# Kernel tuning notes

Measured on AMD Instinct MI355X. Metric: run time of the kernel, lower is better.

The kernel has to match this reference:

```python
import jax, jax.numpy as jnp
import numpy as np

B, N, D, H, HID = 8, 729, 1152, 12, 4304
HD = D // H
EPS = 1e-6


def _layer_norm(x, g, b):
    mu = jnp.mean(x, axis=-1, keepdims=True)
    var = jnp.mean((x - mu) ** 2, axis=-1, keepdims=True)
    return (x - mu) / jnp.sqrt(var + EPS) * g + b


def setup_inputs() -> dict:
    key = jax.random.key(0)
    ks = jax.random.split(key, 9)
    s = 0.02
    return {
        "x": jax.random.normal(ks[0], (B, N, D), jnp.float32),
        "wq": jax.random.normal(ks[1], (D, D), jnp.float32) * s,
        "bq": jnp.zeros((D,), jnp.float32),
        "wk": jax.random.normal(ks[2], (D, D), jnp.float32) * s,
        "bk": jnp.zeros((D,), jnp.float32),
        "wv": jax.random.normal(ks[3], (D, D), jnp.float32) * s,
        "bv": jnp.zeros((D,), jnp.float32),
        "wo": jax.random.normal(ks[4], (D, D), jnp.float32) * s,
        "bo": jnp.zeros((D,), jnp.float32),
        "ln1_g": jnp.ones((D,), jnp.float32),
        "ln1_b": jnp.zeros((D,), jnp.float32),
        "w_fc1": jax.random.normal(ks[5], (HID, D), jnp.float32) * s,
        "b_fc1": jnp.zeros((HID,), jnp.float32),
        "w_fc2": jax.random.normal(ks[6], (D, HID), jnp.float32) * s,
        "b_fc2": jnp.zeros((D,), jnp.float32),
        "ln2_g": jnp.ones((D,), jnp.float32),
        "ln2_b": jnp.zeros((D,), jnp.float32),
    }


def reference(x, wq, bq, wk, bk, wv, bv, wo, bo, ln1_g, ln1_b,
              w_fc1, b_fc1, w_fc2, b_fc2, ln2_g, ln2_b):
    b, n, d = x.shape
    # split_heads in the source is a plain view (B, H, N, HD) -- NOT a transpose.
    def heads(t):
        return t.reshape(b, H, n, HD)

    Q = heads(x @ wq.T + bq)
    K = heads(x @ wk.T + bk)
    V = heads(x @ wv.T + bv)

    scores = jnp.einsum("bhqd,bhkd->bhqk", Q, K) * (HD ** -0.5)
    attn_w = jax.nn.softmax(scores, axis=-1)
    o = jnp.einsum("bhqk,bhkd->bhqd", attn_w, V)  # [B,H,N,HD]
    o = jnp.swapaxes(o, 1, 2).reshape(b, n, d)
    attn_out = o @ wo.T + bo

    # post-norm: LN(sublayer) + residual
    h = _layer_norm(attn_out, ln1_g, ln1_b) + x

    # quirky MLP: activation applied BEFORE fc1 (faithful to source)
    m = jax.nn.gelu(h, approximate=True)
    m = m @ w_fc1.T + b_fc1
    m = m @ w_fc2.T + b_fc2

    return _layer_norm(m, ln2_g, ln2_b) + h
```

## Files before the change

### kernel.cpp

```cpp
#include <hip/hip_runtime.h>
#include <hip/hip_bf16.h>

#define BF16 __hip_bfloat16

typedef short short8 __attribute__((ext_vector_type(8)));
typedef short short4v __attribute__((ext_vector_type(4)));
typedef float v4f __attribute__((ext_vector_type(4)));
typedef float f4 __attribute__((ext_vector_type(4)));

__device__ float g_bp[1152];
__device__ BF16  g_wm[1152 * 1152];

__device__ __forceinline__ short f2bs(float f) {
    __hip_bfloat16 h = __float2bfloat16(f);
    return *(short*)&h;
}

__device__ __forceinline__ float bs2f(short s) {
    __hip_bfloat16 h = *(__hip_bfloat16*)&s;
    return __bfloat162float(h);
}

__device__ __forceinline__ void async_cp16(const BF16* g, BF16* l) {
    __builtin_amdgcn_global_load_lds(
        (const __attribute__((address_space(1))) void*)g,
        (__attribute__((address_space(3))) void*)l,
        16, 0, 0);
}

__global__ __launch_bounds__(256) void prep_kernel(
    const float* __restrict__ wq, const float* __restrict__ wk,
    const float* __restrict__ wv, const float* __restrict__ wo,
    const float* __restrict__ wfc1, const float* __restrict__ wfc2,
    const float* __restrict__ x,
    const float* __restrict__ bfc1, const float* __restrict__ bfc2,
    BF16* __restrict__ wbq, BF16* __restrict__ wbk,
    BF16* __restrict__ wbv, BF16* __restrict__ wbo,
    BF16* __restrict__ wbf1t, BF16* __restrict__ wbf2,
    BF16* __restrict__ xb)
{
    __shared__ float tile[64][65];
    const int bid = blockIdx.x;
    const int tid = threadIdx.x;

    if (bid < 16641) {
        const int i = bid * 256 + tid;
        constexpr int N_DD  = 331776;
        constexpr int N4    = 4 * N_DD;
        constexpr int N_F2  = 1253376;
        constexpr int E_F2  = N4 + N_F2;
        constexpr int N_X   = 1679616;
        constexpr int TOTAL = E_F2 + N_X;

        if (i < N4) {
            int seg = i / N_DD, j = i - seg * N_DD;
            const float* s = (seg == 0) ? wq : (seg == 1) ? wk : (seg == 2) ? wv : wo;
            BF16* d = (seg == 0) ? wbq : (seg == 1) ? wbk : (seg == 2) ? wbv : wbo;
            f4 v = ((const f4*)s)[j];
            short4v o = {f2bs(v.x), f2bs(v.y), f2bs(v.z), f2bs(v.w)};
            ((short4v*)d)[j] = o;
        } else if (i < E_F2) {
            int j = i - N4;
            int row = j / 1088;
            int c = (j - row * 1088) * 4;
            short4v o = {0, 0, 0, 0};
            if (c < 4304) {
                f4 v = *(const f4*)(wfc2 + (size_t)row * 4304 + c);
                o[0] = f2bs(v.x); o[1] = f2bs(v.y); o[2] = f2bs(v.z); o[3] = f2bs(v.w);
            }
            *(short4v*)(wbf2 + (size_t)row * 4352 + c) = o;
        } else if (i < TOTAL) {
            int j = i - E_F2;
            f4 v = ((const f4*)x)[j];
            short4v o = {f2bs(v.x), f2bs(v.y), f2bs(v.z), f2bs(v.w)};
            ((short4v*)xb)[j] = o;
        }
    } else if (bid < 17865) {
        const int b2 = bid - 16641;
        const int h0 = (b2 % 68) * 64;
        const int d0 = (b2 / 68) * 64;
#pragma unroll
        for (int i = 0; i < 4; ++i) {
            int lin = tid + i * 256;
            int r = lin >> 4, c4 = lin & 15;
            f4 v = {0.f, 0.f, 0.f, 0.f};
            if (h0 + r < 4304)
                v = *(const f4*)(wfc1 + (size_t)(h0 + r) * 1152 + d0 + c4 * 4);
            tile[r][c4 * 4 + 0] = v.x;
            tile[r][c4 * 4 + 1] = v.y;
            tile[r][c4 * 4 + 2] = v.z;
            tile[r][c4 * 4 + 3] = v.w;
        }
        __syncthreads();
#pragma unroll
        for (int i = 0; i < 2; ++i) {
            int lin = tid + i * 256;
            int dr = lin >> 3, h8 = lin & 7;
            short8 o;
#pragma unroll
            for (int e = 0; e < 8; ++e)
                o[e] = f2bs(tile[h8 * 8 + e][dr]);
            *(short8*)(wbf1t + (size_t)(d0 + dr) * 4352 + h0 + h8 * 8) = o;
        }
    } else {
        const int row = (bid - 17865) * 4 + (tid >> 6);
        const int lane = tid & 63;
        const float* wr = wfc2 + (size_t)row * 4304;
        float s = 0.f;
        for (int k = lane; k < 4304; k += 64) s += wr[k] * bfc1[k];
#pragma unroll
        for (int mm = 1; mm < 64; mm <<= 1) s += __shfl_xor(s, mm, 64);
        if (lane == 0) g_bp[row] = s + bfc2[row];
    }
}

__global__ __launch_bounds__(256) void qkv_wm_kernel(
    const BF16* __restrict__ A,
    const BF16* __restrict__ Wqkv,
    const float* __restrict__ b0, const float* __restrict__ b1,
    const float* __restrict__ b2,
    BF16* __restrict__ C, size_t cstride, int M,
    const BF16* __restrict__ W2,
    const BF16* __restrict__ W1t)
{
    __shared__ __align__(16) BF16 smem[256 * 64];
    const int bid  = blockIdx.x;
    const int tid  = threadIdx.x;
    const int lane = tid & 63;
    const int wave = tid >> 6;
    const int quad = lane >> 4;
    const int l16  = lane & 15;
    const int wm   = (wave >> 1) * 64;
    const int wn   = (wave & 1) * 64;
    const v4f zf = {0.f, 0.f, 0.f, 0.f};
    BF16* As = smem;
    BF16* Bs = smem + 128 * 64;

    v4f acc[4][4];
#pragma unroll
    for (int i = 0; i < 4; ++i)
#pragma unroll
        for (int j = 0; j < 4; ++j) acc[i][j] = zf;

    if (bid < 81) {
        const int m0 = (bid % 9) * 128;
        const int n0 = (bid / 9) * 128;

        const BF16* gA[4]; BF16* lA[4];
        const BF16* gB[4]; BF16* lB[4];
#pragma unroll
        for (int i = 0; i < 4; ++i) {
            int c = tid + i * 256;
            int src = ((((c & 7) - (c >> 3)) & 7) << 3);
            gA[i] = W2 + (size_t)(m0 + (c >> 3)) * 4352 + src;
            gB[i] = W1t + (size_t)(n0 + (c >> 3)) * 4352 + src;
            lA[i] = As + (c & ~63) * 8;
            lB[i] = Bs + (c & ~63) * 8;
        }

        for (int kt = 0; kt < 68; ++kt) {
#pragma unroll
            for (int i = 0; i < 4; ++i) { async_cp16(gA[i], lA[i]); gA[i] += 64; }
#pragma unroll
            for (int i = 0; i < 4; ++i) { async_cp16(gB[i], lB[i]); gB[i] += 64; }
            __syncthreads();
#pragma unroll
            for (int ks = 0; ks < 2; ++ks) {
                short8 af[4], bfg[4];
#pragma unroll
                for (int mt = 0; mt < 4; ++mt) {
                    int row = wm + mt * 16 + l16;
                    af[mt] = *(const short8*)(As + row * 64 + ((((ks << 2) | quad) + row & 7) & 7) * 8);
                }
#pragma unroll
                for (int nt = 0; nt < 4; ++nt) {
                    int row = wn + nt * 16 + l16;
                    bfg[nt] = *(const short8*)(Bs + row * 64 + ((((ks << 2) | quad) + row & 7) & 7) * 8);
                }
#pragma unroll
                for (int mt = 0; mt < 4; ++mt)
#pragma unroll
                    for (int nt = 0; nt < 4; ++nt)
                        acc[mt][nt] = __builtin_amdgcn_mfma_f32_16x16x32_bf16(
                            af[mt], bfg[nt], acc[mt][nt], 0, 0, 0);
            }
            __syncthreads();
        }

#pragma unroll
        for (int mt = 0; mt < 4; ++mt)
#pragma unroll
            for (int nt = 0; nt < 4; ++nt)
#pragma unroll
                for (int r2 = 0; r2 < 4; ++r2) {
                    int row_l = wm + mt * 16 + quad * 4 + r2;
                    int col_l = wn + nt * 16 + l16;
                    smem[row_l * 128 + col_l] = __float2bfloat16(acc[mt][nt][r2]);
                }
        __syncthreads();
#pragma unroll
        for (int p = 0; p < 8; ++p) {
            int idx = p * 256 + tid;
            *(short8*)(g_wm + (size_t)(m0 + (idx >> 4)) * 1152 + n0 + (idx & 15) * 8) =
                *(const short8*)(smem + idx * 8);
        }
    } else {
        const int id2 = bid - 81;
        const int m0 = (id2 % 46) * 128;
        const int n0 = (id2 / 46) * 128;

        const BF16* gA[4]; BF16* lA[4];
        const BF16* gB[4]; BF16* lB[4];
#pragma unroll
        for (int i = 0; i < 4; ++i) {
            int c = tid + i * 256;
            int src = ((((c & 7) - (c >> 3)) & 7) << 3);
            gA[i] = A + (size_t)(m0 + (c >> 3)) * 1152 + src;
            gB[i] = Wqkv + (size_t)(n0 + (c >> 3)) * 1152 + src;
            lA[i] = As + (c & ~63) * 8;
            lB[i] = Bs + (c & ~63) * 8;
        }

        for (int kt = 0; kt < 18; ++kt) {
#pragma unroll
            for (int i = 0; i < 4; ++i) { async_cp16(gA[i], lA[i]); gA[i] += 64; }
#pragma unroll
            for (int i = 0; i < 4; ++i) { async_cp16(gB[i], lB[i]); gB[i] += 64; }
            __syncthreads();
#pragma unroll
            for (int ks = 0; ks < 2; ++ks) {
                short8 af[4], bfg[4];
#pragma unroll
                for (int mt = 0; mt < 4; ++mt) {
                    int row = wm + mt * 16 + l16;
                    af[mt] = *(const short8*)(As + row * 64 + ((((ks << 2) | quad) + row & 7) & 7) * 8);
                }
#pragma unroll
                for (int nt = 0; nt < 4; ++nt) {
                    int row = wn + nt * 16 + l16;
                    bfg[nt] = *(const short8*)(Bs + row * 64 + ((((ks << 2) | quad) + row & 7) & 7) * 8);
                }
#pragma unroll
                for (int mt = 0; mt < 4; ++mt)
#pragma unroll
                    for (int nt = 0; nt < 4; ++nt)
                        acc[mt][nt] = __builtin_amdgcn_mfma_f32_16x16x32_bf16(
                            af[mt], bfg[nt], acc[mt][nt], 0, 0, 0);
            }
            __syncthreads();
        }

        const int sel = n0 / 1152;
        const float* bp = (sel == 0) ? b0 : (sel == 1) ? b1 : b2;
        BF16* Cb = C + (size_t)sel * cstride;
        const int nl0 = n0 - sel * 1152;

        float bv[4];
#pragma unroll
        for (int nt = 0; nt < 4; ++nt)
            bv[nt] = bp[nl0 + wn + nt * 16 + l16];
#pragma unroll
        for (int mt = 0; mt < 4; ++mt)
#pragma unroll
            for (int nt = 0; nt < 4; ++nt)
#pragma unroll
                for (int r2 = 0; r2 < 4; ++r2) {
                    int row_l = wm + mt * 16 + quad * 4 + r2;
                    int col_l = wn + nt * 16 + l16;
                    smem[row_l * 128 + col_l] = __float2bfloat16(acc[mt][nt][r2] + bv[nt]);
                }
        __syncthreads();
#pragma unroll
        for (int p = 0; p < 8; ++p) {
            int idx = p * 256 + tid;
            int row = m0 + (idx >> 4);
            if (row < M)
                *(short8*)(Cb + (size_t)row * 1152 + nl0 + (idx & 15) * 8) =
                    *(const short8*)(smem + idx * 8);
        }
    }
}

__global__ __launch_bounds__(256) void trans_kernel(
    const BF16* __restrict__ V, BF16* __restrict__ VT)
{
    __shared__ __align__(16) BF16 tl[64][128];
    const int bid = blockIdx.x, tid = threadIdx.x;
    const short8 zero8 = {0, 0, 0, 0, 0, 0, 0, 0};

    if (bid < 1152) {
        const int hg = bid / 12, kb = bid - hg * 12;
        const int b = hg / 12, hh = hg - b * 12;
        const BF16* src = V + (size_t)b * 839808 + (size_t)hh * 69984;
        BF16* dst = VT + (size_t)hg * 86016;
        const int kk0 = kb * 64;
#pragma unroll
        for (int i = 0; i < 3; ++i) {
            int c = tid + i * 256;
            int r = c / 12, cg = c - r * 12;
            short8 v = (kk0 + r < 729)
                ? *(const short8*)(src + (size_t)(kk0 + r) * 96 + cg * 8) : zero8;
            *(short8*)(&tl[r][(cg ^ ((r >> 3) & 7)) * 8]) = v;
        }
        __syncthreads();
#pragma unroll
        for (int i = 0; i < 3; ++i) {
            int wc = tid + i * 256;
            int hd = wc >> 3, o = wc & 7;
            int sp = (((hd >> 3) ^ o) << 3) + (hd & 7);
            short8 out;
#pragma unroll
            for (int j = 0; j < 8; ++j)
                out[j] = *(const short*)&tl[o * 8 + j][sp];
            *(short8*)(dst + (size_t)hd * 768 + kk0 + o * 8) = out;
        }
    } else {
        int c = (bid - 1152) * 256 + tid;
        int hg = c / 1536, rem = c - hg * 1536;
        int r = rem / 96, ock = rem - r * 96;
        int kk = ock * 8;
        short8 v = zero8;
        if (r == 0) {
            const short oneb = 0x3F80;
#pragma unroll
            for (int j = 0; j < 8; ++j) v[j] = (kk + j < 729) ? oneb : (short)0;
        }
        *(short8*)(VT + (size_t)hg * 86016 + (size_t)(96 + r) * 768 + kk) = v;
    }
}

template<int TM>
__global__ __launch_bounds__(256) void gemm_bt_t(
    const BF16* __restrict__ A, int lda,
    const BF16* __restrict__ W, int ldb,
    const float* __restrict__ bias, int nbias,
    BF16* __restrict__ C, int ldc,
    int M, int Kr)
{
    constexpr int MT = TM / 32;
    __shared__ __align__(16) BF16 smem[(TM + 128) * 64];
    BF16* As = smem;
    BF16* Bs = smem + TM * 64;

    const int tid  = threadIdx.x;
    const int lane = tid & 63;
    const int wave = tid >> 6;
    const int quad = lane >> 4;
    const int l16  = lane & 15;
    const int wm   = (wave >> 1) * (TM / 2);
    const int wn   = (wave & 1) * 64;
    const int m0   = blockIdx.x * TM;
    const int n0   = blockIdx.y * 128;
    if (m0 >= M) return;

    const v4f zf = {0.f, 0.f, 0.f, 0.f};
    v4f acc[MT][4];
#pragma unroll
    for (int i = 0; i < MT; ++i)
#pragma unroll
        for (int j = 0; j < 4; ++j) acc[i][j] = zf;

    const BF16* gA[MT]; BF16* lA[MT];
#pragma unroll
    for (int i = 0; i < MT; ++i) {
        int c = tid + i * 256;
        gA[i] = A + (size_t)(m0 + (c >> 3)) * lda + ((((c & 7) - (c >> 3)) & 7) << 3);
        lA[i] = As + (c & ~63) * 8;
    }
    const BF16* gB[4]; BF16* lB[4];
#pragma unroll
    for (int i = 0; i < 4; ++i) {
        int c = tid + i * 256;
        gB[i] = W + (size_t)(n0 + (c >> 3)) * ldb + ((((c & 7) - (c >> 3)) & 7) << 3);
        lB[i] = Bs + (c & ~63) * 8;
    }

    const int nk = Kr >> 6;
    for (int kt = 0; kt < nk; ++kt) {
#pragma unroll
        for (int i = 0; i < MT; ++i) { async_cp16(gA[i], lA[i]); gA[i] += 64; }
#pragma unroll
        for (int i = 0; i < 4; ++i)  { async_cp16(gB[i], lB[i]); gB[i] += 64; }
        __syncthreads();

#pragma unroll
        for (int ks = 0; ks < 2; ++ks) {
            short8 af[MT], bfg[4];
#pragma unroll
            for (int mt = 0; mt < MT; ++mt) {
                int row = wm + mt * 16 + l16;
                af[mt] = *(const short8*)(As + row * 64 + ((((ks << 2) | quad) + row & 7) & 7) * 8);
            }
#pragma unroll
            for (int nt = 0; nt < 4; ++nt) {
                int row = wn + nt * 16 + l16;
                bfg[nt] = *(const short8*)(Bs + row * 64 + ((((ks << 2) | quad) + row & 7) & 7) * 8);
            }
#pragma unroll
            for (int mt = 0; mt < MT; ++mt)
#pragma unroll
                for (int nt = 0; nt < 4; ++nt)
                    acc[mt][nt] = __builtin_amdgcn_mfma_f32_16x16x32_bf16(
                        af[mt], bfg[nt], acc[mt][nt], 0, 0, 0);
        }
        __syncthreads();
    }

    float bv[4];
#pragma unroll
    for (int nt = 0; nt < 4; ++nt) {
        int col = n0 + wn + nt * 16 + l16;
        bv[nt] = (col < nbias) ? bias[col] : 0.f;
    }
#pragma unroll
    for (int mt = 0; mt < MT; ++mt)
#pragma unroll
        for (int nt = 0; nt < 4; ++nt)
#pragma unroll
            for (int r2 = 0; r2 < 4; ++r2) {
                int row_l = wm + mt * 16 + quad * 4 + r2;
                int col_l = wn + nt * 16 + l16;
                smem[row_l * 128 + col_l] = __float2bfloat16(acc[mt][nt][r2] + bv[nt]);
            }
    __syncthreads();
#pragma unroll
    for (int p = 0; p < TM / 16; ++p) {
        int idx = p * 256 + tid;
        int row = m0 + (idx >> 4);
        if (row < M)
            *(short8*)(C + (size_t)row * ldc + n0 + (idx & 15) * 8) =
                *(const short8*)(smem + idx * 8);
    }
}

__global__ __launch_bounds__(256) void attn_flash3(
    const BF16* __restrict__ Q, const BF16* __restrict__ K,
    const BF16* __restrict__ VT, BF16* __restrict__ O)
{
    constexpr int NQ = 729, HDk = 96, DM = 1152, LDV = 768;
    __shared__ __align__(16) BF16 Ks[64 * 104];
    __shared__ __align__(16) BF16 Vs[112 * 64];
    __shared__ __align__(16) BF16 Ps[4][32 * 64];

    const int id = blockIdx.x;
    const int xcd = id & 7, slot = id >> 3;
    const int hb = slot / 6, qt = slot - hb * 6;
    const int hg = xcd * 12 + hb;
    const int b = hg / 12, hh = hg - b * 12;

    const int tid = threadIdx.x, wave = tid >> 6, lane = tid & 63;
    const int quad = lane >> 4, l16 = lane & 15;
    const size_t kbase = (size_t)b * (NQ * DM) + (size_t)hh * (NQ * HDk);
    const size_t vbase = (size_t)hg * 112 * LDV;

    const short8 zero8 = {0, 0, 0, 0, 0, 0, 0, 0};
    const v4f zf = {0.f, 0.f, 0.f, 0.f};
    const float C2 = 0.14724445f;

    const int q0w = qt * 128 + wave * 32;
    short8 aq[2][3];
#pragma unroll
    for (int mt = 0; mt < 2; ++mt) {
        int qrow = q0w + mt * 16 + l16;
#pragma unroll
        for (int ks = 0; ks < 3; ++ks)
            aq[mt][ks] = (qrow < NQ)
                ? *(const short8*)(Q + kbase + (size_t)qrow * HDk + ks * 32 + quad * 8)
                : zero8;
    }

    int kk_[3], kg_[3];
#pragma unroll
    for (int i = 0; i < 3; ++i) {
        int c = tid + i * 256;
        kk_[i] = c / 12; kg_[i] = c - kk_[i] * 12;
    }
    int vq_[4], vgr_[4], vhd_[4];
#pragma unroll
    for (int i = 0; i < 4; ++i) {
        int q = wave + 4 * i;
        vq_[i] = q;
        int hd = q * 8 + (lane >> 3);
        vhd_[i] = hd;
        vgr_[i] = ((lane & 7) - hd) & 7;
    }

    v4f oacc[2][7];
#pragma unroll
    for (int mt = 0; mt < 2; ++mt)
#pragma unroll
        for (int nt = 0; nt < 7; ++nt) oacc[mt][nt] = zf;

    for (int kt = 0; kt < 12; ++kt) {
        const int k0 = kt * 64;
#pragma unroll
        for (int i = 0; i < 4; ++i) {
            if (vq_[i] < 14)
                async_cp16(VT + vbase + (size_t)vhd_[i] * LDV + k0 + vgr_[i] * 8,
                           Vs + vq_[i] * 512);
        }
#pragma unroll
        for (int i = 0; i < 3; ++i) {
            short8 v = *(const short8*)(K + kbase + (size_t)(k0 + kk_[i]) * HDk + kg_[i] * 8);
            *(short8*)(Ks + kk_[i] * 104 + kg_[i] * 8) = v;
        }
        __syncthreads();

        v4f s[2][4];
#pragma unroll
        for (int mt = 0; mt < 2; ++mt)
#pragma unroll
            for (int nt = 0; nt < 4; ++nt) s[mt][nt] = zf;
#pragma unroll
        for (int ks = 0; ks < 3; ++ks)
#pragma unroll
            for (int nt = 0; nt < 4; ++nt) {
                short8 bk = *(const short8*)(Ks + (nt * 16 + l16) * 104 + ks * 32 + quad * 8);
#pragma unroll
                for (int mt = 0; mt < 2; ++mt)
                    s[mt][nt] = __builtin_amdgcn_mfma_f32_16x16x32_bf16(
                        aq[mt][ks], bk, s[mt][nt], 0, 0, 0);
            }

        BF16* Pw = &Ps[wave][0];
#pragma unroll
        for (int mt = 0; mt < 2; ++mt)
#pragma unroll
            for (int nt = 0; nt < 4; ++nt)
#pragma unroll
                for (int r = 0; r < 4; ++r)
                    Pw[((mt * 16 + quad * 4 + r) << 6)
                       + ((((nt << 1) | (l16 >> 3)) ^ (quad << 1)) << 3)
                       + (l16 & 7)] =
                        __float2bfloat16(exp2f(s[mt][nt][r] * C2));
        asm volatile("s_waitcnt lgkmcnt(0)" ::: "memory");

        short8 ap[2][2];
#pragma unroll
        for (int mt = 0; mt < 2; ++mt)
#pragma unroll
            for (int kc = 0; kc < 2; ++kc)
                ap[mt][kc] = *(const short8*)(Pw + ((mt * 16 + l16) << 6)
                    + ((((kc << 2) | quad) ^ (((l16 >> 2) & 3) << 1)) << 3));
#pragma unroll
        for (int nt = 0; nt < 7; ++nt) {
            int hd = nt * 16 + l16;
#pragma unroll
            for (int kc = 0; kc < 2; ++kc) {
                short8 bv = *(const short8*)(Vs + hd * 64 + (((kc * 4 + quad) + hd & 7) & 7) * 8);
#pragma unroll
                for (int mt = 0; mt < 2; ++mt)
                    oacc[mt][nt] = __builtin_amdgcn_mfma_f32_16x16x32_bf16(
                        ap[mt][kc], bv, oacc[mt][nt], 0, 0, 0);
            }
        }
        __syncthreads();
    }

#pragma unroll
    for (int mt = 0; mt < 2; ++mt) {
        const int qb = q0w + mt * 16 + quad * 4;
#pragma unroll
        for (int r = 0; r < 4; ++r) {
            int q = qb + r;
            float lv = __shfl(oacc[mt][6][r], quad << 4, 64);
            float inv = (lv > 0.f) ? 1.f / lv : 0.f;
            if (q >= NQ) continue;
#pragma unroll
            for (int nt = 0; nt < 6; ++nt)
                O[(size_t)b * (NQ * DM) + (size_t)q * DM + hh * HDk + nt * 16 + l16] =
                    __float2bfloat16(oacc[mt][nt][r] * inv);
        }
    }
}

__device__ __forceinline__ float block_sum256(float v, float* red, int tid)
{
#pragma unroll
    for (int mm = 1; mm < 64; mm <<= 1) v += __shfl_xor(v, mm, 64);
    if ((tid & 63) == 0) red[tid >> 6] = v;
    __syncthreads();
    float r = red[0] + red[1] + red[2] + red[3];
    __syncthreads();
    return r;
}

__global__ __launch_bounds__(256) void ln1_gelu_kernel(
    const BF16* __restrict__ ao, const float* __restrict__ x,
    const float* __restrict__ gw, const float* __restrict__ bw,
    BF16* __restrict__ hout, BF16* __restrict__ gout)
{
    __shared__ float red[4];
    const int row = blockIdx.x, tid = threadIdx.x;
    const bool act = tid < 144;
    float v[8];
    float s = 0.f;
    if (act) {
        short8 pk = ((const short8*)(ao + (size_t)row * 1152))[tid];
#pragma unroll
        for (int j = 0; j < 8; ++j) { v[j] = bs2f(pk[j]); s += v[j]; }
    } else {
#pragma unroll
        for (int j = 0; j < 8; ++j) v[j] = 0.f;
    }
    s = block_sum256(s, red, tid);
    float mu = s * (1.f / 1152.f);
    float vsum = 0.f;
    if (act) {
#pragma unroll
        for (int j = 0; j < 8; ++j) { float d = v[j] - mu; vsum += d * d; }
    }
    vsum = block_sum256(vsum, red, tid);
    float rstd = rsqrtf(vsum * (1.f / 1152.f) + 1e-6f);
    if (act) {
        f4 g0 = ((const f4*)gw)[2 * tid], g1 = ((const f4*)gw)[2 * tid + 1];
        f4 b0 = ((const f4*)bw)[2 * tid], b1 = ((const f4*)bw)[2 * tid + 1];
        const f4* xr = (const f4*)(x + (size_t)row * 1152);
        f4 x0 = xr[2 * tid], x1 = xr[2 * tid + 1];
        short8 ho, go;
#pragma unroll
        for (int j = 0; j < 8; ++j) {
            float gj = (j < 4) ? g0[j] : g1[j - 4];
            float bj = (j < 4) ? b0[j] : b1[j - 4];
            float xj = (j < 4) ? x0[j] : x1[j - 4];
            float hv = (v[j] - mu) * rstd * gj + bj + xj;
            ho[j] = f2bs(hv);
            float t = hv;
            float gl = 0.5f * t * (1.f + tanhf(0.7978845608028654f * (t + 0.044715f * t * t * t)));
            go[j] = f2bs(gl);
        }
        ((short8*)(hout + (size_t)row * 1152))[tid] = ho;
        ((short8*)(gout + (size_t)row * 1152))[tid] = go;
    }
}

__global__ __launch_bounds__(256) void ln2_kernel(
    const BF16* __restrict__ m2, const BF16* __restrict__ hf,
    const float* __restrict__ gw, const float* __restrict__ bw,
    float* __restrict__ out)
{
    __shared__ float red[4];
    const int row = blockIdx.x, tid = threadIdx.x;
    const bool act = tid < 144;
    float v[8];
    float s = 0.f;
    if (act) {
        short8 pk = ((const short8*)(m2 + (size_t)row * 1152))[tid];
#pragma unroll
        for (int j = 0; j < 8; ++j) { v[j] = bs2f(pk[j]); s += v[j]; }
    } else {
#pragma unroll
        for (int j = 0; j < 8; ++j) v[j] = 0.f;
    }
    s = block_sum256(s, red, tid);
    float mu = s * (1.f / 1152.f);
    float vsum = 0.f;
    if (act) {
#pragma unroll
        for (int j = 0; j < 8; ++j) { float d = v[j] - mu; vsum += d * d; }
    }
    vsum = block_sum256(vsum, red, tid);
    float rstd = rsqrtf(vsum * (1.f / 1152.f) + 1e-6f);
    if (act) {
        f4 g0 = ((const f4*)gw)[2 * tid], g1 = ((const f4*)gw)[2 * tid + 1];
        f4 b0 = ((const f4*)bw)[2 * tid], b1 = ((const f4*)bw)[2 * tid + 1];
        short8 hfv = ((const short8*)(hf + (size_t)row * 1152))[tid];
        f4 o0, o1;
#pragma unroll
        for (int j = 0; j < 8; ++j) {
            float gj = (j < 4) ? g0[j] : g1[j - 4];
            float bj = (j < 4) ? b0[j] : b1[j - 4];
            float ov = (v[j] - mu) * rstd * gj + bj + bs2f(hfv[j]);
            if (j < 4) o0[j] = ov; else o1[j - 4] = ov;
        }
        f4* orow = (f4*)(out + (size_t)row * 1152);
        orow[2 * tid] = o0;
        orow[2 * tid + 1] = o1;
    }
}

extern "C" void kernel_launch(void* const* d_in, const int* in_sizes, int n_in,
                              void* d_out, int out_size, void* d_ws, size_t ws_size,
                              hipStream_t stream)
{
    const float* x    = (const float*)d_in[0];
    const float* wq   = (const float*)d_in[1];
    const float* bq   = (const float*)d_in[2];
    const float* wk   = (const float*)d_in[3];
    const float* bk   = (const float*)d_in[4];
    const float* wv   = (const float*)d_in[5];
    const float* bv   = (const float*)d_in[6];
    const float* wo   = (const float*)d_in[7];
    const float* bo   = (const float*)d_in[8];
    const float* ln1g = (const float*)d_in[9];
    const float* ln1b = (const float*)d_in[10];
    const float* wfc1 = (const float*)d_in[11];
    const float* bfc1 = (const float*)d_in[12];
    const float* wfc2 = (const float*)d_in[13];
    const float* bfc2 = (const float*)d_in[14];
    const float* ln2g = (const float*)d_in[15];
    const float* ln2b = (const float*)d_in[16];

    const int T = 8 * 729;
    const int D = 1152, HIDP = 4352;
    const size_t TD = (size_t)T * D;
    const size_t WDD = (size_t)D * D;

    BF16* wbq   = (BF16*)d_ws;
    BF16* wbk   = wbq + WDD;
    BF16* wbv   = wbk + WDD;
    BF16* wbo   = wbv + WDD;
    BF16* wbf1t = wbo + WDD;
    BF16* wbf2  = wbf1t + (size_t)HIDP * D;
    BF16* xb    = wbf2 + (size_t)D * HIDP;
    BF16* S0    = xb + TD;
    BF16* S1    = S0 + TD;
    BF16* S2    = S1 + TD;
    BF16* S3    = S2 + TD;
    BF16* C0    = S3 + TD;
    BF16* C1    = C0 + TD;
    BF16* VT    = C0;

    static float* bp_dev = nullptr;
    static BF16*  wm_dev = nullptr;
    if (!bp_dev) hipGetSymbolAddress((void**)&bp_dev, HIP_SYMBOL(g_bp));
    if (!wm_dev) hipGetSymbolAddress((void**)&wm_dev, HIP_SYMBOL(g_wm));

    dim3 blk(256);

    prep_kernel<<<18153, blk, 0, stream>>>(
        wq, wk, wv, wo, wfc1, wfc2, x, bfc1, bfc2,
        wbq, wbk, wbv, wbo, wbf1t, wbf2, xb);

    qkv_wm_kernel<<<1323, blk, 0, stream>>>(
        xb, wbq, bq, bk, bv, S0, TD, T, wbf2, wbf1t);

    trans_kernel<<<1728, blk, 0, stream>>>(S2, VT);

    attn_flash3<<<576, blk, 0, stream>>>(S0, S1, VT, S3);

    gemm_bt_t<64><<<dim3(92, 9), blk, 0, stream>>>(S3, D, wbo, D, bo, D, C0, D, T, D);

    ln1_gelu_kernel<<<T, blk, 0, stream>>>(C0, x, ln1g, ln1b, C1, C0);

    gemm_bt_t<64><<<dim3(92, 9), blk, 0, stream>>>(C0, D, wm_dev, D, bp_dev, D, S3, D, T, D);

    ln2_kernel<<<T, blk, 0, stream>>>(S3, C1, ln2g, ln2b, (float*)d_out);
}
```

Before: 397.1 us.

## Remap GEMM workgroups per XCD and prefetch K tiles in attention

GEMM launches become 1D grids, and a chunked XCD mapping gives each XCD a contiguous range of tiles. The intent is better L2 reuse of A and W rows on the multi-die GPU. In the attention kernel, the next K tile is loaded into registers while the current tile is computed. The old __syncthreads calls are split into explicit waitcnt and barrier pairs so the V async copy can overlap the QK and softmax work. This adds register pressure, and the hand-placed waitcnt counts must be correct.

```diff
diff --git a/kernel.cpp b/kernel.cpp
--- a/kernel.cpp
+++ b/kernel.cpp
@@ -26,6 +26,12 @@
         (const __attribute__((address_space(1))) void*)g,
         (__attribute__((address_space(3))) void*)l,
         16, 0, 0);
+}
+
+__device__ __forceinline__ int xcd_chunk(int u, int nwg) {
+    int xcd = u & 7, i = u >> 3;
+    int q = nwg >> 3, r = nwg & 7;
+    return (xcd < r ? xcd * (q + 1) : r * (q + 1) + (xcd - r) * q) + i;
 }
 
 __global__ __launch_bounds__(256) void prep_kernel(
@@ -205,9 +211,9 @@
                 *(const short8*)(smem + idx * 8);
         }
     } else {
-        const int id2 = bid - 81;
-        const int m0 = (id2 % 46) * 128;
-        const int n0 = (id2 / 46) * 128;
+        const int wg = xcd_chunk(bid - 81, 1242);
+        const int m0 = (wg / 27) * 128;
+        const int n0 = (wg % 27) * 128;
 
         const BF16* gA[4]; BF16* lA[4];
         const BF16* gB[4]; BF16* lB[4];
@@ -335,7 +341,7 @@
     const BF16* __restrict__ W, int ldb,
     const float* __restrict__ bias, int nbias,
     BF16* __restrict__ C, int ldc,
-    int M, int Kr)
+    int M, int Kr, int nbn)
 {
     constexpr int MT = TM / 32;
     __shared__ __align__(16) BF16 smem[(TM + 128) * 64];
@@ -349,8 +355,9 @@
     const int l16  = lane & 15;
     const int wm   = (wave >> 1) * (TM / 2);
     const int wn   = (wave & 1) * 64;
-    const int m0   = blockIdx.x * TM;
-    const int n0   = blockIdx.y * 128;
+    const int wg   = xcd_chunk(blockIdx.x, gridDim.x);
+    const int m0   = (wg / nbn) * TM;
+    const int n0   = (wg % nbn) * 128;
     if (m0 >= M) return;
 
     const v4f zf = {0.f, 0.f, 0.f, 0.f};
@@ -491,20 +498,31 @@
 #pragma unroll
         for (int nt = 0; nt < 7; ++nt) oacc[mt][nt] = zf;
 
+    short8 kreg[3];
+#pragma unroll
+    for (int i = 0; i < 3; ++i)
+        kreg[i] = *(const short8*)(K + kbase + (size_t)kk_[i] * HDk + kg_[i] * 8);
+
     for (int kt = 0; kt < 12; ++kt) {
         const int k0 = kt * 64;
+#pragma unroll
+        for (int i = 0; i < 3; ++i)
+            *(short8*)(Ks + kk_[i] * 104 + kg_[i] * 8) = kreg[i];
 #pragma unroll
         for (int i = 0; i < 4; ++i) {
             if (vq_[i] < 14)
                 async_cp16(VT + vbase + (size_t)vhd_[i] * LDV + k0 + vgr_[i] * 8,
                            Vs + vq_[i] * 512);
         }
-#pragma unroll
-        for (int i = 0; i < 3; ++i) {
-            short8 v = *(const short8*)(K + kbase + (size_t)(k0 + kk_[i]) * HDk + kg_[i] * 8);
-            *(short8*)(Ks + kk_[i] * 104 + kg_[i] * 8) = v;
-        }
-        __syncthreads();
+        asm volatile("s_waitcnt lgkmcnt(0)" ::: "memory");
+        __builtin_amdgcn_s_barrier();
+        __builtin_amdgcn_sched_barrier(0);
+        {
+            const int kn = (kt < 11) ? (k0 + 64) : 0;
+#pragma unroll
+            for (int i = 0; i < 3; ++i)
+                kreg[i] = *(const short8*)(K + kbase + (size_t)(kn + kk_[i]) * HDk + kg_[i] * 8);
+        }
 
         v4f s[2][4];
 #pragma unroll
@@ -542,6 +560,11 @@
             for (int kc = 0; kc < 2; ++kc)
                 ap[mt][kc] = *(const short8*)(Pw + ((mt * 16 + l16) << 6)
                     + ((((kc << 2) | quad) ^ (((l16 >> 2) & 3) << 1)) << 3));
+
+        asm volatile("s_waitcnt vmcnt(3)" ::: "memory");
+        __builtin_amdgcn_s_barrier();
+        __builtin_amdgcn_sched_barrier(0);
+
 #pragma unroll
         for (int nt = 0; nt < 7; ++nt) {
             int hd = nt * 16 + l16;
@@ -554,7 +577,9 @@
                         ap[mt][kc], bv, oacc[mt][nt], 0, 0, 0);
             }
         }
-        __syncthreads();
+        asm volatile("s_waitcnt lgkmcnt(0)" ::: "memory");
+        __builtin_amdgcn_s_barrier();
+        __builtin_amdgcn_sched_barrier(0);
     }
 
 #pragma unroll
@@ -739,11 +764,11 @@
 
     attn_flash3<<<576, blk, 0, stream>>>(S0, S1, VT, S3);
 
-    gemm_bt_t<64><<<dim3(92, 9), blk, 0, stream>>>(S3, D, wbo, D, bo, D, C0, D, T, D);
+    gemm_bt_t<64><<<828, blk, 0, stream>>>(S3, D, wbo, D, bo, D, C0, D, T, D, 9);
 
     ln1_gelu_kernel<<<T, blk, 0, stream>>>(C0, x, ln1g, ln1b, C1, C0);
 
-    gemm_bt_t<64><<<dim3(92, 9), blk, 0, stream>>>(C0, D, wm_dev, D, bp_dev, D, S3, D, T, D);
+    gemm_bt_t<64><<<828, blk, 0, stream>>>(C0, D, wm_dev, D, bp_dev, D, S3, D, T, D, 9);
 
     ln2_kernel<<<T, blk, 0, stream>>>(S3, C1, ln2g, ln2b, (float*)d_out);
 }
```

Measured after the change: 387.0 us. 2.5% less time.
